# Kernel tuning notes

Measured on AMD Instinct MI355X. Metric: run time of the kernel, lower is better.

## Reference

```python
import jax, jax.numpy as jnp
import numpy as np

B, C, H, W, S = 32, 512, 32, 32, 4
HW = H * W
OUT = HW // S  # conv1/conv2 out channels = 256
EPS = 1e-5


def setup_inputs() -> dict:
    key = jax.random.key(0)
    ks = jax.random.split(key, 8)
    d = {}
    d["x"] = jax.random.normal(ks[0], (B, C, H, W), jnp.float32)
    # conv1 / bn1 (operate on x_flat with 'channels' = h*w)
    d["w1"] = jax.random.normal(ks[1], (OUT, HW), jnp.float32) * 0.02
    d["b1"] = jnp.zeros((OUT,), jnp.float32)
    d["g1"] = jnp.ones((OUT,), jnp.float32)
    d["be1"] = jnp.zeros((OUT,), jnp.float32)
    d["m1"] = jax.random.normal(ks[2], (OUT,), jnp.float32) * 0.01
    d["v1"] = jnp.ones((OUT,), jnp.float32)
    # conv2 / bn2
    d["w2"] = jax.random.normal(ks[3], (OUT, HW), jnp.float32) * 0.02
    d["b2"] = jnp.zeros((OUT,), jnp.float32)
    d["g2"] = jnp.ones((OUT,), jnp.float32)
    d["be2"] = jnp.zeros((OUT,), jnp.float32)
    d["m2"] = jax.random.normal(ks[4], (OUT,), jnp.float32) * 0.01
    d["v2"] = jnp.ones((OUT,), jnp.float32)
    # conv3 / bn3 (1x1 conv on the real channel dim c)
    d["w3"] = jax.random.normal(ks[5], (C, C), jnp.float32) * 0.02
    d["b3"] = jnp.zeros((C,), jnp.float32)
    d["g3"] = jnp.ones((C,), jnp.float32)
    d["be3"] = jnp.zeros((C,), jnp.float32)
    d["m3"] = jax.random.normal(ks[6], (C,), jnp.float32) * 0.01
    d["v3"] = jnp.ones((C,), jnp.float32)
    # conv4: 1x1 conv mapping 1+2c channels -> 1
    d["w4"] = jax.random.normal(ks[7], (1 + 2 * C,), jnp.float32) * 0.02
    d["b4"] = jnp.zeros((), jnp.float32)
    return d


def _bn1d(t, g, be, m, v):
    # t: [b, o, c]; BatchNorm (eval mode) over channel axis 1
    scale = g / jnp.sqrt(v + EPS)
    return (t - m[:, None]) * scale[:, None] + be[:, None]


def reference(x, w1, b1, g1, be1, m1, v1,
              w2, b2, g2, be2, m2, v2,
              w3, b3, g3, be3, m3, v3,
              w4, b4):
    b, c, h, w = x.shape
    # x_flat: [b, h*w, c] -- conv1/conv2 are 1x1 convs over 'channels' = h*w
    xf = x.reshape(b, c, h * w).transpose(0, 2, 1)
    theta = jax.nn.relu(_bn1d(jnp.einsum('oq,bqc->boc', w1, xf) + b1[:, None],
                              g1, be1, m1, v1))  # [b, OUT, c]
    phi = jax.nn.relu(_bn1d(jnp.einsum('oq,bqc->boc', w2, xf) + b2[:, None],
                            g2, be2, m2, v2))    # [b, OUT, c]
    # per-batch conv2d-as-matmul loop collapses to one batched GEMM:
    # affinity[b, i, j] = sum_k phi[b, k, i] * theta[b, k, j]
    aff = jnp.einsum('bki,bkj->bij', phi, theta)  # [b, c, c]
    # x_embed: 1x1 conv + BN + ReLU + global average pool -> [b, c]
    scale3 = g3 / jnp.sqrt(v3 + EPS)
    xe = jnp.einsum('oc,bchw->bohw', w3, x) + b3[:, None, None]
    xe = jax.nn.relu((xe - m3[:, None, None]) * scale3[:, None, None]
                     + be3[:, None, None])
    xe = xe.mean(axis=(2, 3))  # [b, c]
    # conv4 over y = cat([x_embed, affinity_a, affinity_b], dim=1):
    # affinity_a[b,i,0,p] = aff[b,i,p]; affinity_b[b,i,0,p] = aff[b,p,i]
    logits = (w4[0] * xe
              + jnp.einsum('i,bip->bp', w4[1:1 + c], aff)
              + jnp.einsum('i,bpi->bp', w4[1 + c:], aff)
              + b4)
    a = jax.nn.sigmoid(logits)  # [b, c]
    return x * a[:, :, None, None]
```

## Files before the change

kernel.cpp:

```cpp
#include <hip/hip_runtime.h>
#include <math.h>

#define BB   32
#define CC   512
#define HWW  1024
#define OUTC 256
#define EPSV 1e-5f

typedef __attribute__((ext_vector_type(8))) short bfrag;
typedef __attribute__((ext_vector_type(4))) float f32x4;
typedef __attribute__((ext_vector_type(4))) unsigned int u32x4;

__device__ inline unsigned short f2bf(float x){
  unsigned int uu = __float_as_uint(x);
  uu += 0x7fff + ((uu >> 16) & 1);
  return (unsigned short)(uu >> 16);
}
__device__ inline float bf2f(unsigned short h){
  return __uint_as_float(((unsigned int)h) << 16);
}
__device__ inline void packpair(float v0, float v1, unsigned int& hw, unsigned int& lw){
  unsigned short h0 = f2bf(v0), h1 = f2bf(v1);
  unsigned short l0 = f2bf(v0 - bf2f(h0)), l1 = f2bf(v1 - bf2f(h1));
  hw = (unsigned int)h0 | ((unsigned int)h1 << 16);
  lw = (unsigned int)l0 | ((unsigned int)l1 << 16);
}

#define ASYNC16(g, l) \
  __builtin_amdgcn_global_load_lds((const __attribute__((address_space(1))) unsigned int*)(g), \
                                   (__attribute__((address_space(3))) unsigned int*)(l), 16, 0, 0)
#define WAITV(N) asm volatile("s_waitcnt vmcnt(" #N ")" ::: "memory")


__global__ __launch_bounds__(256) void prep(
    const float* __restrict__ x,
    const float* __restrict__ w1, const float* __restrict__ w2,
    const float* __restrict__ w3,
    unsigned short* __restrict__ Xhi, unsigned short* __restrict__ Xlo,
    unsigned short* __restrict__ XThi,
    unsigned short* __restrict__ Whi, unsigned short* __restrict__ Wlo,
    unsigned short* __restrict__ W3hi,
    float* __restrict__ accz)
{
  const int tid = threadIdx.x;
  if (blockIdx.z == 32) {
    int worker = (blockIdx.y * 16 + blockIdx.x) * 256 + tid;
    accz[worker] = 0.f;
#pragma unroll
    for (int s = 0; s < 2; ++s) {
      int cid  = worker * 2 + s;
      int tile = cid >> 6, l = cid & 63;
      int o = (tile >> 5) * 16 + (l & 15);
      int k = (tile & 31) * 32 + (l >> 4) * 8;
      const float* src = (o < 256) ? (w1 + (size_t)o * 1024 + k)
                                   : (w2 + (size_t)(o - 256) * 1024 + k);
      u32x4 hv, lv;
#pragma unroll
      for (int j = 0; j < 4; ++j) {
        unsigned int hw, lw;
        packpair(src[2 * j], src[2 * j + 1], hw, lw);
        hv[j] = hw; lv[j] = lw;
      }
      size_t base = (size_t)tile * 512 + (size_t)l * 8;
      *(u32x4*)(Whi + base) = hv;
      *(u32x4*)(Wlo + base) = lv;
    }
    {
      int tile = worker >> 6, l = worker & 63;
      int o = (tile >> 4) * 16 + (l & 15);
      int c = (tile & 15) * 32 + (l >> 4) * 8;
      const float* src = w3 + (size_t)o * 512 + c;
      u32x4 hv;
#pragma unroll
      for (int j = 0; j < 4; ++j) {
        unsigned short h0 = f2bf(src[2 * j]), h1 = f2bf(src[2 * j + 1]);
        hv[j] = (unsigned int)h0 | ((unsigned int)h1 << 16);
      }
      *(u32x4*)(W3hi + (size_t)tile * 512 + (size_t)l * 8) = hv;
    }
    return;
  }
  __shared__ float T[64][65];
  const int b = blockIdx.z, c0 = blockIdx.y * 64, p0 = blockIdx.x * 64;
  const int tr = tid >> 4, tc4 = (tid & 15) * 4;
  const float* xb = x + (size_t)b * 524288;
#pragma unroll
  for (int r = 0; r < 4; ++r) {
    int cl = tr + r * 16;
    float4 v = *(const float4*)(xb + (size_t)(c0 + cl) * 1024 + p0 + tc4);
    T[cl][tc4 + 0] = v.x; T[cl][tc4 + 1] = v.y;
    T[cl][tc4 + 2] = v.z; T[cl][tc4 + 3] = v.w;
  }
  __syncthreads();
#pragma unroll
  for (int s = 0; s < 2; ++s) {
    int cid  = tid + s * 256;
    int tile = cid >> 6, l = cid & 63;
    int tileC = tile >> 1, tileP = tile & 1;
    int cl = tileC * 16 + (l & 15);
    int pl = tileP * 32 + (l >> 4) * 8;
    u32x4 hv, lv;
#pragma unroll
    for (int j = 0; j < 4; ++j) {
      unsigned int hw, lw;
      packpair(T[cl][pl + 2 * j], T[cl][pl + 2 * j + 1], hw, lw);
      hv[j] = hw; lv[j] = lw;
    }
    size_t base = (size_t)b * 524288
                + ((size_t)((c0 + cl) >> 4) * 32 + (size_t)((p0 + pl) >> 5)) * 512
                + (size_t)l * 8;
    *(u32x4*)(Xhi + base) = hv;
    *(u32x4*)(Xlo + base) = lv;
  }
#pragma unroll
  for (int s = 0; s < 2; ++s) {
    int cid  = tid + s * 256;
    int tile = cid >> 6, l = cid & 63;
    int tileP = tile >> 1, tileC = tile & 1;
    int pl = tileP * 16 + (l & 15);
    int cl = tileC * 32 + (l >> 4) * 8;
    u32x4 hv;
#pragma unroll
    for (int j = 0; j < 4; ++j) {
      unsigned short h0 = f2bf(T[cl + 2 * j][pl]);
      unsigned short h1 = f2bf(T[cl + 2 * j + 1][pl]);
      hv[j] = (unsigned int)h0 | ((unsigned int)h1 << 16);
    }
    size_t base = (size_t)b * 524288
                + ((size_t)((p0 + pl) >> 4) * 16 + (size_t)((c0 + cl) >> 5)) * 512
                + (size_t)l * 8;
    *(u32x4*)(XThi + base) = hv;
  }
}

__global__ __launch_bounds__(256, 2) void gemm_fused(
    const unsigned short* __restrict__ Xhi, const unsigned short* __restrict__ Xlo,
    const unsigned short* __restrict__ Whi, const unsigned short* __restrict__ Wlo,
    const unsigned short* __restrict__ W3hi, const unsigned short* __restrict__ XThi,
    const float* __restrict__ b1p, const float* __restrict__ g1p,
    const float* __restrict__ be1p, const float* __restrict__ m1p, const float* __restrict__ v1p,
    const float* __restrict__ b2p, const float* __restrict__ g2p,
    const float* __restrict__ be2p, const float* __restrict__ m2p, const float* __restrict__ v2p,
    const float* __restrict__ b3p, const float* __restrict__ g3p,
    const float* __restrict__ be3p, const float* __restrict__ m3p, const float* __restrict__ v3p,
    const float* __restrict__ w4,
    float* __restrict__ P2, float* __restrict__ u, float* __restrict__ t,
    float* __restrict__ xe_acc)
{
  __shared__ unsigned short smem[32768];
  const int fid  = blockIdx.x;
  const int tid  = threadIdx.x;
  const int wave = tid >> 6, lane = tid & 63;
  const int fr = lane & 15, fq = lane >> 4;

  if (fid < 512) {
    const int xcd = fid & 7;
    const int n0  = ((fid >> 3) & 3) * 128;
    const int bc  = ((fid >> 5) << 3) | xcd;
    const int b   = bc >> 2;
    const int c0  = (bc & 3) * 128;
    const int wm = wave & 1, wn = wave >> 1;

    const unsigned short* gsrc;
    int ldst;
    if (wave == 0)      { gsrc = Xhi + (size_t)b * 524288 + (size_t)(c0 >> 4) * 16384; ldst = 0; }
    else if (wave == 1) { gsrc = Xlo + (size_t)b * 524288 + (size_t)(c0 >> 4) * 16384; ldst = 4096; }
    else if (wave == 2) { gsrc = Whi + (size_t)(n0 >> 4) * 16384; ldst = 8192; }
    else                { gsrc = Wlo + (size_t)(n0 >> 4) * 16384; ldst = 12288; }
    gsrc += (size_t)lane * 8;

    f32x4 acc[4][4];
    const f32x4 zz = {0.f, 0.f, 0.f, 0.f};
#pragma unroll
    for (int i = 0; i < 4; ++i)
#pragma unroll
      for (int j = 0; j < 4; ++j) acc[i][j] = zz;

#pragma unroll
    for (int i = 0; i < 8; ++i)
      ASYNC16(gsrc + (size_t)i * 16384, smem + ldst + i * 512);

    int cur = 0;
    for (int kq = 0; kq < 32; ++kq) {
      __builtin_amdgcn_sched_barrier(0);
      if (kq + 1 < 32) {
        unsigned short* nb = smem + (cur ^ 1) * 16384 + ldst;
#pragma unroll
        for (int i = 0; i < 8; ++i)
          ASYNC16(gsrc + (size_t)i * 16384 + (kq + 1) * 512, nb + i * 512);
        WAITV(8);
      } else {
        WAITV(0);
      }
      __builtin_amdgcn_s_barrier();
      __builtin_amdgcn_sched_barrier(0);

      const unsigned short* bufc = smem + cur * 16384;
      bfrag ah[4], al[4], bh[4], bl[4];
#pragma unroll
      for (int i = 0; i < 4; ++i) {
        ah[i] = *(const bfrag*)&bufc[(wm * 4 + i) * 512 + lane * 8];
        al[i] = *(const bfrag*)&bufc[4096 + (wm * 4 + i) * 512 + lane * 8];
      }
#pragma unroll
      for (int j = 0; j < 4; ++j) {
        bh[j] = *(const bfrag*)&bufc[8192 + (wn * 4 + j) * 512 + lane * 8];
        bl[j] = *(const bfrag*)&bufc[12288 + (wn * 4 + j) * 512 + lane * 8];
      }
#pragma unroll
      for (int i = 0; i < 4; ++i)
#pragma unroll
        for (int j = 0; j < 4; ++j) {
          acc[i][j] = __builtin_amdgcn_mfma_f32_16x16x32_bf16(ah[i], bh[j], acc[i][j], 0, 0, 0);
          acc[i][j] = __builtin_amdgcn_mfma_f32_16x16x32_bf16(ah[i], bl[j], acc[i][j], 0, 0, 0);
          acc[i][j] = __builtin_amdgcn_mfma_f32_16x16x32_bf16(al[i], bh[j], acc[i][j], 0, 0, 0);
        }
      __builtin_amdgcn_sched_barrier(0);
      __builtin_amdgcn_s_barrier();
      cur ^= 1;
    }
    __builtin_amdgcn_sched_barrier(0);

    const float *bias, *gg, *bes, *mm, *vv_; int cof;
    if (n0 < 256) { bias = b1p; gg = g1p; bes = be1p; mm = m1p; vv_ = v1p; cof = 0; }
    else          { bias = b2p; gg = g2p; bes = be2p; mm = m2p; vv_ = v2p; cof = 256; }
    const float* wsel = (n0 < 256) ? (w4 + 513) : (w4 + 1);
    float* dsel = (n0 < 256) ? (t + b * 256) : (u + b * 256);
    const int cobase = (n0 - cof) + wn * 64;
    float wt[4][4];
#pragma unroll
    for (int i = 0; i < 4; ++i)
#pragma unroll
      for (int r = 0; r < 4; ++r)
        wt[i][r] = wsel[c0 + wm * 64 + i * 16 + fq * 4 + r];

#pragma unroll
    for (int j = 0; j < 4; ++j) {
      int co = n0 + wn * 64 + j * 16 + fr;
      int q = co - cof;
      float s  = gg[q] * rsqrtf(vv_[q] + EPSV);
      float sh = (bias[q] - mm[q]) * s + bes[q];
      float psum = 0.f;
#pragma unroll
      for (int i = 0; i < 4; ++i) {
        int crow = c0 + wm * 64 + i * 16 + fq * 4;
        float* dst = P2 + ((size_t)b * 512 + crow) * 512 + co;
#pragma unroll
        for (int r = 0; r < 4; ++r) {
          float val = fmaxf(acc[i][j][r] * s + sh, 0.f);
          dst[(size_t)r * 512] = val;
          psum += wt[i][r] * val;
        }
      }
      psum += __shfl_xor(psum, 16);
      psum += __shfl_xor(psum, 32);
      if (fq == 0) atomicAdd(&dsel[cobase + j * 16 + fr], psum);
    }
  } else {
    const int h  = fid - 512;
    const int n0 = (h & 7) * 128;
    const int m0 = ((h >> 3) & 3) * 128;
    const int b  = h >> 5;
    const int wm = wave & 1, wn = wave >> 1;

    const unsigned short* gsrc;
    int ldst;
    if (wave < 2) { gsrc = W3hi + (size_t)((m0 >> 4) + wave * 4) * 8192; ldst = wave * 2048; }
    else { gsrc = XThi + (size_t)b * 524288 + (size_t)((n0 >> 4) + (wave - 2) * 4) * 8192;
           ldst = 4096 + (wave - 2) * 2048; }
    gsrc += (size_t)lane * 8;

    f32x4 acc[4][4];
    const f32x4 zz = {0.f, 0.f, 0.f, 0.f};
#pragma unroll
    for (int i = 0; i < 4; ++i)
#pragma unroll
      for (int j = 0; j < 4; ++j) acc[i][j] = zz;

#pragma unroll
    for (int i = 0; i < 4; ++i)
      ASYNC16(gsrc + (size_t)i * 8192, smem + ldst + i * 512);

    int cur = 0;
    for (int kq = 0; kq < 16; ++kq) {
      __builtin_amdgcn_sched_barrier(0);
      if (kq + 1 < 16) {
        unsigned short* nb = smem + (cur ^ 1) * 8192 + ldst;
#pragma unroll
        for (int i = 0; i < 4; ++i)
          ASYNC16(gsrc + (size_t)i * 8192 + (kq + 1) * 512, nb + i * 512);
        WAITV(4);
      } else {
        WAITV(0);
      }
      __builtin_amdgcn_s_barrier();
      __builtin_amdgcn_sched_barrier(0);

      const unsigned short* bufc = smem + cur * 8192;
      bfrag af[4], bf4[4];
#pragma unroll
      for (int i = 0; i < 4; ++i)
        af[i] = *(const bfrag*)&bufc[(wm * 4 + i) * 512 + lane * 8];
#pragma unroll
      for (int j = 0; j < 4; ++j)
        bf4[j] = *(const bfrag*)&bufc[4096 + (wn * 4 + j) * 512 + lane * 8];
#pragma unroll
      for (int i = 0; i < 4; ++i)
#pragma unroll
        for (int j = 0; j < 4; ++j)
          acc[i][j] = __builtin_amdgcn_mfma_f32_16x16x32_bf16(af[i], bf4[j], acc[i][j], 0, 0, 0);
      __builtin_amdgcn_sched_barrier(0);
      __builtin_amdgcn_s_barrier();
      cur ^= 1;
    }
    __builtin_amdgcn_sched_barrier(0);

#pragma unroll
    for (int i = 0; i < 4; ++i) {
#pragma unroll
      for (int r = 0; r < 4; ++r) {
        int o = m0 + wm * 64 + i * 16 + fq * 4 + r;
        float s  = g3p[o] * rsqrtf(v3p[o] + EPSV);
        float sh = (b3p[o] - m3p[o]) * s + be3p[o];
        float v = fmaxf(acc[i][0][r] * s + sh, 0.f) + fmaxf(acc[i][1][r] * s + sh, 0.f)
                + fmaxf(acc[i][2][r] * s + sh, 0.f) + fmaxf(acc[i][3][r] * s + sh, 0.f);
        v += __shfl_xor(v, 1); v += __shfl_xor(v, 2);
        v += __shfl_xor(v, 4); v += __shfl_xor(v, 8);
        if (fr == 0) atomicAdd(&xe_acc[b * 512 + o], v);
      }
    }
  }
}

__global__ __launch_bounds__(256) void k4_gate_out(
    const float* __restrict__ P2, const float* __restrict__ u,
    const float* __restrict__ t, const float* __restrict__ xe_acc,
    const float* __restrict__ w4, const float* __restrict__ b4,
    const float* __restrict__ x, float* __restrict__ out)
{
  __shared__ float us[256], ts[256];
  const int b = blockIdx.x;
  us[threadIdx.x] = u[b * 256 + threadIdx.x];
  ts[threadIdx.x] = t[b * 256 + threadIdx.x];
  __syncthreads();
  const int wave = threadIdx.x >> 6, lane = threadIdx.x & 63;
  const int p = blockIdx.y * 4 + wave;
  const float* row = P2 + ((size_t)b * 512 + p) * 512;
  float4 th = *(const float4*)&row[lane * 4];
  float4 ph = *(const float4*)&row[256 + lane * 4];
  int ki = lane * 4;
  float rs = th.x * us[ki] + th.y * us[ki + 1] + th.z * us[ki + 2] + th.w * us[ki + 3]
           + ph.x * ts[ki] + ph.y * ts[ki + 1] + ph.z * ts[ki + 2] + ph.w * ts[ki + 3];
  rs += __shfl_xor(rs, 1);  rs += __shfl_xor(rs, 2);  rs += __shfl_xor(rs, 4);
  rs += __shfl_xor(rs, 8);  rs += __shfl_xor(rs, 16); rs += __shfl_xor(rs, 32);
  float xe = xe_acc[b * 512 + p] * (1.f / 1024.f);
  float logit = w4[0] * xe + rs + b4[0];
  float a = 1.f / (1.f + expf(-logit));
  const float4* xr = (const float4*)(x + ((size_t)b * 512 + p) * 1024);
  float4* orow = (float4*)(out + ((size_t)b * 512 + p) * 1024);
#pragma unroll
  for (int r2 = 0; r2 < 4; ++r2) {
    float4 xv = xr[lane + r2 * 64];
    float4 ov; ov.x = xv.x * a; ov.y = xv.y * a; ov.z = xv.z * a; ov.w = xv.w * a;
    orow[lane + r2 * 64] = ov;
  }
}

__global__ __launch_bounds__(256) void k1_theta_phi(
    const float* __restrict__ x,
    const float* __restrict__ w1, const float* __restrict__ b1,
    const float* __restrict__ g1, const float* __restrict__ be1,
    const float* __restrict__ m1, const float* __restrict__ v1,
    const float* __restrict__ w2, const float* __restrict__ b2,
    const float* __restrict__ g2, const float* __restrict__ be2,
    const float* __restrict__ m2, const float* __restrict__ v2,
    float* __restrict__ P)
{
  __shared__ __align__(16) float Ws[32][68];
  __shared__ __align__(16) float Xs[32][68];
  const int b  = blockIdx.z;
  const int o0 = blockIdx.y * 64;
  const int c0 = blockIdx.x * 64;
  const int tid = threadIdx.x;
  const int tx = tid & 15, ty = tid >> 4;
  const float* __restrict__ Wbase = (o0 < OUTC) ? (w1 + (size_t)o0 * HWW)
                                                : (w2 + (size_t)(o0 - OUTC) * HWW);
  const float* __restrict__ xb = x + (size_t)b * CC * HWW;
  float acc[4][4] = {{0.f}};
  for (int k0 = 0; k0 < HWW; k0 += 32) {
#pragma unroll
    for (int r = 0; r < 2; ++r) {
      int id  = tid + (r << 8);
      int row = id >> 3;
      int cg  = (id & 7) << 2;
      float4 wv = *(const float4*)(Wbase + (size_t)row * HWW + k0 + cg);
      Ws[cg+0][row] = wv.x; Ws[cg+1][row] = wv.y; Ws[cg+2][row] = wv.z; Ws[cg+3][row] = wv.w;
      float4 xv = *(const float4*)(xb + (size_t)(c0 + row) * HWW + k0 + cg);
      Xs[cg+0][row] = xv.x; Xs[cg+1][row] = xv.y; Xs[cg+2][row] = xv.z; Xs[cg+3][row] = xv.w;
    }
    __syncthreads();
#pragma unroll
    for (int k = 0; k < 32; ++k) {
      float4 av = *(const float4*)&Ws[k][ty * 4];
      float4 bv = *(const float4*)&Xs[k][tx * 4];
      acc[0][0] += av.x*bv.x; acc[0][1] += av.x*bv.y; acc[0][2] += av.x*bv.z; acc[0][3] += av.x*bv.w;
      acc[1][0] += av.y*bv.x; acc[1][1] += av.y*bv.y; acc[1][2] += av.y*bv.z; acc[1][3] += av.y*bv.w;
      acc[2][0] += av.z*bv.x; acc[2][1] += av.z*bv.y; acc[2][2] += av.z*bv.z; acc[2][3] += av.z*bv.w;
      acc[3][0] += av.w*bv.x; acc[3][1] += av.w*bv.y; acc[3][2] += av.w*bv.z; acc[3][3] += av.w*bv.w;
    }
    __syncthreads();
  }
  const float *bias, *g, *be, *m, *v; int ob;
  if (o0 < OUTC) { bias = b1; g = g1; be = be1; m = m1; v = v1; ob = o0; }
  else           { bias = b2; g = g2; be = be2; m = m2; v = v2; ob = o0 - OUTC; }
#pragma unroll
  for (int i = 0; i < 4; ++i) {
    int oi = ob + ty * 4 + i;
    float sc = g[oi] * rsqrtf(v[oi] + EPSV);
    float sh = be[oi] - m[oi] * sc;
    float bb = bias[oi];
    float4 ov;
    ov.x = fmaxf((acc[i][0] + bb) * sc + sh, 0.f);
    ov.y = fmaxf((acc[i][1] + bb) * sc + sh, 0.f);
    ov.z = fmaxf((acc[i][2] + bb) * sc + sh, 0.f);
    ov.w = fmaxf((acc[i][3] + bb) * sc + sh, 0.f);
    int oo = o0 + ty * 4 + i;
    *(float4*)(P + ((size_t)b * 512 + oo) * 512 + c0 + tx * 4) = ov;
  }
}

__global__ __launch_bounds__(256) void k2_xe(
    const float* __restrict__ x, const float* __restrict__ w3,
    const float* __restrict__ b3, const float* __restrict__ g3,
    const float* __restrict__ be3, const float* __restrict__ m3,
    const float* __restrict__ v3, float* __restrict__ xe_acc)
{
  __shared__ __align__(16) float As[32][68];
  __shared__ __align__(16) float Bs[32][68];
  const int b  = blockIdx.z;
  const int o0 = blockIdx.y * 64;
  const int p0 = blockIdx.x * 64;
  const int tid = threadIdx.x;
  const int tx = tid & 15, ty = tid >> 4;
  const float* __restrict__ xb = x + (size_t)b * CC * HWW;
  float acc[4][4] = {{0.f}};
  for (int ck = 0; ck < CC; ck += 32) {
#pragma unroll
    for (int r = 0; r < 2; ++r) {
      int id  = tid + (r << 8);
      int row = id >> 3;
      int cg  = (id & 7) << 2;
      float4 wv = *(const float4*)(w3 + (size_t)(o0 + row) * CC + ck + cg);
      As[cg+0][row] = wv.x; As[cg+1][row] = wv.y; As[cg+2][row] = wv.z; As[cg+3][row] = wv.w;
      int brow = id >> 4;
      int pg   = (id & 15) << 2;
      float4 xv = *(const float4*)(xb + (size_t)(ck + brow) * HWW + p0 + pg);
      *(float4*)&Bs[brow][pg] = xv;
    }
    __syncthreads();
#pragma unroll
    for (int k = 0; k < 32; ++k) {
      float4 av = *(const float4*)&As[k][ty * 4];
      float4 bv = *(const float4*)&Bs[k][tx * 4];
      acc[0][0] += av.x*bv.x; acc[0][1] += av.x*bv.y; acc[0][2] += av.x*bv.z; acc[0][3] += av.x*bv.w;
      acc[1][0] += av.y*bv.x; acc[1][1] += av.y*bv.y; acc[1][2] += av.y*bv.z; acc[1][3] += av.y*bv.w;
      acc[2][0] += av.z*bv.x; acc[2][1] += av.z*bv.y; acc[2][2] += av.z*bv.z; acc[2][3] += av.z*bv.w;
      acc[3][0] += av.w*bv.x; acc[3][1] += av.w*bv.y; acc[3][2] += av.w*bv.z; acc[3][3] += av.w*bv.w;
    }
    __syncthreads();
  }
#pragma unroll
  for (int i = 0; i < 4; ++i) {
    int oo = o0 + ty * 4 + i;
    float sc = g3[oo] * rsqrtf(v3[oo] + EPSV);
    float sh = be3[oo] - m3[oo] * sc;
    float bb = b3[oo];
    float ps = fmaxf((acc[i][0] + bb) * sc + sh, 0.f)
             + fmaxf((acc[i][1] + bb) * sc + sh, 0.f)
             + fmaxf((acc[i][2] + bb) * sc + sh, 0.f)
             + fmaxf((acc[i][3] + bb) * sc + sh, 0.f);
    ps += __shfl_xor(ps, 1);
    ps += __shfl_xor(ps, 2);
    ps += __shfl_xor(ps, 4);
    ps += __shfl_xor(ps, 8);
    if (tx == 0) atomicAdd(&xe_acc[b * CC + oo], ps);
  }
}

__global__ __launch_bounds__(256) void k3_ut(
    const float* __restrict__ P, const float* __restrict__ w4,
    float* __restrict__ u, float* __restrict__ t)
{
  const int b = blockIdx.x;
  const int wv = threadIdx.x >> 6, lane = threadIdx.x & 63;
  const int k = blockIdx.y * 4 + wv;
  const float* __restrict__ w4a = w4 + 1;
  const float* __restrict__ w4b = w4 + 1 + CC;
  const float* __restrict__ throw_ = P + ((size_t)b * 512 + k) * 512;
  const float* __restrict__ phrow  = P + ((size_t)b * 512 + 256 + k) * 512;
  float su = 0.f, st = 0.f;
#pragma unroll
  for (int i = lane; i < CC; i += 64) {
    su += w4a[i] * phrow[i];
    st += w4b[i] * throw_[i];
  }
#pragma unroll
  for (int off = 32; off > 0; off >>= 1) {
    su += __shfl_down(su, off);
    st += __shfl_down(st, off);
  }
  if (lane == 0) { u[b * OUTC + k] = su; t[b * OUTC + k] = st; }
}

__global__ __launch_bounds__(256) void k4_gate(
    const float* __restrict__ P, const float* __restrict__ u,
    const float* __restrict__ t, const float* __restrict__ xe_acc,
    const float* __restrict__ w4, const float* __restrict__ b4,
    float* __restrict__ amul)
{
  __shared__ float us[256], ts[256];
  const int b = blockIdx.x;
  const int p = blockIdx.y * 256 + threadIdx.x;
  us[threadIdx.x] = u[b * OUTC + threadIdx.x];
  ts[threadIdx.x] = t[b * OUTC + threadIdx.x];
  __syncthreads();
  const float* __restrict__ theta = P + (size_t)b * 512 * 512;
  const float* __restrict__ phi   = theta + 256 * 512;
  float r = 0.f, s = 0.f;
#pragma unroll 8
  for (int k = 0; k < OUTC; ++k) {
    r += us[k] * theta[(size_t)k * 512 + p];
    s += ts[k] * phi[(size_t)k * 512 + p];
  }
  float xe = xe_acc[b * CC + p] * (1.0f / 1024.0f);
  float logit = w4[0] * xe + r + s + b4[0];
  amul[b * CC + p] = 1.0f / (1.0f + expf(-logit));
}

__global__ __launch_bounds__(256) void k5_out(
    const float* __restrict__ x, const float* __restrict__ amul,
    float* __restrict__ out)
{
  int i = blockIdx.x * 256 + threadIdx.x;
  float4 xv = ((const float4*)x)[i];
  float a = amul[i >> 8];
  float4 ov; ov.x = xv.x * a; ov.y = xv.y * a; ov.z = xv.z * a; ov.w = xv.w * a;
  ((float4*)out)[i] = ov;
}

extern "C" void kernel_launch(void* const* d_in, const int* in_sizes, int n_in,
                              void* d_out, int out_size, void* d_ws, size_t ws_size,
                              hipStream_t stream)
{
  (void)in_sizes; (void)n_in; (void)out_size;
  const float* x   = (const float*)d_in[0];
  const float* w1  = (const float*)d_in[1];
  const float* b1  = (const float*)d_in[2];
  const float* g1  = (const float*)d_in[3];
  const float* be1 = (const float*)d_in[4];
  const float* m1  = (const float*)d_in[5];
  const float* v1  = (const float*)d_in[6];
  const float* w2  = (const float*)d_in[7];
  const float* b2  = (const float*)d_in[8];
  const float* g2  = (const float*)d_in[9];
  const float* be2 = (const float*)d_in[10];
  const float* m2  = (const float*)d_in[11];
  const float* v2  = (const float*)d_in[12];
  const float* w3  = (const float*)d_in[13];
  const float* b3  = (const float*)d_in[14];
  const float* g3  = (const float*)d_in[15];
  const float* be3 = (const float*)d_in[16];
  const float* m3  = (const float*)d_in[17];
  const float* v3  = (const float*)d_in[18];
  const float* w4  = (const float*)d_in[19];
  const float* b4  = (const float*)d_in[20];
  float* out = (float*)d_out;

  if (ws_size >= 136970240ull) {
    float* P2     = (float*)d_ws;
    float* xe_acc = P2 + 8388608;
    float* u      = P2 + 8404992;
    float* t      = P2 + 8413184;
    unsigned short* Xhi  = (unsigned short*)((char*)d_ws + 33685504);
    unsigned short* Xlo  = Xhi + 16777216;
    unsigned short* XThi = Xlo + 16777216;
    unsigned short* Whi  = XThi + 16777216;
    unsigned short* Wlo  = Whi + 524288;
    unsigned short* W3hi = Wlo + 524288;

    prep<<<dim3(16, 8, 33), 256, 0, stream>>>(x, w1, w2, w3, Xhi, Xlo, XThi,
                                              Whi, Wlo, W3hi, xe_acc);
    gemm_fused<<<dim3(1536), 256, 0, stream>>>(Xhi, Xlo, Whi, Wlo, W3hi, XThi,
        b1, g1, be1, m1, v1, b2, g2, be2, m2, v2, b3, g3, be3, m3, v3,
        w4, P2, u, t, xe_acc);
    k4_gate_out<<<dim3(32, 128), 256, 0, stream>>>(P2, u, t, xe_acc, w4, b4, x, out);
  } else {
    float* P      = (float*)d_ws;
    float* xe_acc = P + (size_t)BB * 512 * 512;
    float* u      = xe_acc + BB * CC;
    float* t      = u + BB * OUTC;
    float* amul   = t + BB * OUTC;

    hipMemsetAsync(xe_acc, 0, (size_t)BB * CC * sizeof(float), stream);

    dim3 blk(256);
    k1_theta_phi<<<dim3(8, 8, BB), blk, 0, stream>>>(x, w1, b1, g1, be1, m1, v1,
                                                     w2, b2, g2, be2, m2, v2, P);
    k2_xe<<<dim3(16, 8, BB), blk, 0, stream>>>(x, w3, b3, g3, be3, m3, v3, xe_acc);
    k3_ut<<<dim3(BB, 64), blk, 0, stream>>>(P, w4, u, t);
    k4_gate<<<dim3(BB, 2), blk, 0, stream>>>(P, u, t, xe_acc, w4, b4, amul);
    k5_out<<<dim3((BB * CC * HWW / 4) / 256), blk, 0, stream>>>(x, amul, out);
  }
}
```

Before: 257.4 us.

## Load weight fragments directly to registers, stage only activations in LDS

In both GEMM branches the weight operand (W hi/lo, W3) is no longer staged through shared memory. Each wave now loads its own fragments straight from global memory into registers, double-buffered across two k-steps. Only the activation tiles still go through LDS, so shared memory per block halves and the loop is manually unrolled by two with fixed buffers. The aim is less LDS traffic and capacity and more blocks resident per CU. The cost is more VGPR pressure and weight data read redundantly from global/L2 by waves that share a column tile.

```diff
diff --git a/kernel.cpp b/kernel.cpp
--- a/kernel.cpp
+++ b/kernel.cpp
@@ -147,7 +147,7 @@
     float* __restrict__ P2, float* __restrict__ u, float* __restrict__ t,
     float* __restrict__ xe_acc)
 {
-  __shared__ unsigned short smem[32768];
+  __shared__ unsigned short smem[16384];
   const int fid  = blockIdx.x;
   const int tid  = threadIdx.x;
   const int wave = tid >> 6, lane = tid & 63;
@@ -161,13 +161,13 @@
     const int c0  = (bc & 3) * 128;
     const int wm = wave & 1, wn = wave >> 1;
 
-    const unsigned short* gsrc;
-    int ldst;
-    if (wave == 0)      { gsrc = Xhi + (size_t)b * 524288 + (size_t)(c0 >> 4) * 16384; ldst = 0; }
-    else if (wave == 1) { gsrc = Xlo + (size_t)b * 524288 + (size_t)(c0 >> 4) * 16384; ldst = 4096; }
-    else if (wave == 2) { gsrc = Whi + (size_t)(n0 >> 4) * 16384; ldst = 8192; }
-    else                { gsrc = Wlo + (size_t)(n0 >> 4) * 16384; ldst = 12288; }
-    gsrc += (size_t)lane * 8;
+    const unsigned short* gAh = Xhi + (size_t)b * 524288
+        + (size_t)((c0 >> 4) + 2 * wave) * 16384 + (size_t)lane * 8;
+    const unsigned short* gAl = Xlo + (size_t)b * 524288
+        + (size_t)((c0 >> 4) + 2 * wave) * 16384 + (size_t)lane * 8;
+
+    const bfrag* Bh = (const bfrag*)Whi + (size_t)((n0 >> 4) + wn * 4) * 2048 + lane;
+    const bfrag* Bl = (const bfrag*)Wlo + (size_t)((n0 >> 4) + wn * 4) * 2048 + lane;
 
     f32x4 acc[4][4];
     const f32x4 zz = {0.f, 0.f, 0.f, 0.f};
@@ -176,48 +176,91 @@
 #pragma unroll
       for (int j = 0; j < 4; ++j) acc[i][j] = zz;
 
-#pragma unroll
-    for (int i = 0; i < 8; ++i)
-      ASYNC16(gsrc + (size_t)i * 16384, smem + ldst + i * 512);
-
-    int cur = 0;
-    for (int kq = 0; kq < 32; ++kq) {
-      __builtin_amdgcn_sched_barrier(0);
-      if (kq + 1 < 32) {
-        unsigned short* nb = smem + (cur ^ 1) * 16384 + ldst;
-#pragma unroll
-        for (int i = 0; i < 8; ++i)
-          ASYNC16(gsrc + (size_t)i * 16384 + (kq + 1) * 512, nb + i * 512);
-        WAITV(8);
+    bfrag bhA[4], blA[4], bhB[4], blB[4];
+#pragma unroll
+    for (int j = 0; j < 4; ++j) {
+      bhA[j] = Bh[(size_t)j * 2048];
+      blA[j] = Bl[(size_t)j * 2048];
+    }
+    __builtin_amdgcn_sched_barrier(0);
+#pragma unroll
+    for (int ti = 0; ti < 2; ++ti) {
+      ASYNC16(gAh + (size_t)ti * 16384, smem + (2 * wave + ti) * 512);
+      ASYNC16(gAl + (size_t)ti * 16384, smem + 4096 + (2 * wave + ti) * 512);
+    }
+
+    for (int kq = 0; kq < 32; kq += 2) {
+      __builtin_amdgcn_sched_barrier(0);
+#pragma unroll
+      for (int j = 0; j < 4; ++j) {
+        bhB[j] = Bh[(size_t)j * 2048 + (kq + 1) * 64];
+        blB[j] = Bl[(size_t)j * 2048 + (kq + 1) * 64];
+      }
+      __builtin_amdgcn_sched_barrier(0);
+#pragma unroll
+      for (int ti = 0; ti < 2; ++ti) {
+        ASYNC16(gAh + (size_t)ti * 16384 + (kq + 1) * 512, smem + 8192 + (2 * wave + ti) * 512);
+        ASYNC16(gAl + (size_t)ti * 16384 + (kq + 1) * 512, smem + 12288 + (2 * wave + ti) * 512);
+      }
+      WAITV(12);
+      __builtin_amdgcn_s_barrier();
+      __builtin_amdgcn_sched_barrier(0);
+      {
+        bfrag ah[4], al[4];
+#pragma unroll
+        for (int i = 0; i < 4; ++i) {
+          ah[i] = *(const bfrag*)&smem[(wm * 4 + i) * 512 + lane * 8];
+          al[i] = *(const bfrag*)&smem[4096 + (wm * 4 + i) * 512 + lane * 8];
+        }
+#pragma unroll
+        for (int i = 0; i < 4; ++i)
+#pragma unroll
+          for (int j = 0; j < 4; ++j) {
+            acc[i][j] = __builtin_amdgcn_mfma_f32_16x16x32_bf16(ah[i], bhA[j], acc[i][j], 0, 0, 0);
+            acc[i][j] = __builtin_amdgcn_mfma_f32_16x16x32_bf16(ah[i], blA[j], acc[i][j], 0, 0, 0);
+            acc[i][j] = __builtin_amdgcn_mfma_f32_16x16x32_bf16(al[i], bhA[j], acc[i][j], 0, 0, 0);
+          }
+      }
+      __builtin_amdgcn_sched_barrier(0);
+      __builtin_amdgcn_s_barrier();
+
+      __builtin_amdgcn_sched_barrier(0);
+      if (kq + 2 < 32) {
+#pragma unroll
+        for (int j = 0; j < 4; ++j) {
+          bhA[j] = Bh[(size_t)j * 2048 + (kq + 2) * 64];
+          blA[j] = Bl[(size_t)j * 2048 + (kq + 2) * 64];
+        }
+        __builtin_amdgcn_sched_barrier(0);
+#pragma unroll
+        for (int ti = 0; ti < 2; ++ti) {
+          ASYNC16(gAh + (size_t)ti * 16384 + (kq + 2) * 512, smem + (2 * wave + ti) * 512);
+          ASYNC16(gAl + (size_t)ti * 16384 + (kq + 2) * 512, smem + 4096 + (2 * wave + ti) * 512);
+        }
+        WAITV(12);
       } else {
         WAITV(0);
       }
       __builtin_amdgcn_s_barrier();
       __builtin_amdgcn_sched_barrier(0);
-
-      const unsigned short* bufc = smem + cur * 16384;
-      bfrag ah[4], al[4], bh[4], bl[4];
-#pragma unroll
-      for (int i = 0; i < 4; ++i) {
-        ah[i] = *(const bfrag*)&bufc[(wm * 4 + i) * 512 + lane * 8];
-        al[i] = *(const bfrag*)&bufc[4096 + (wm * 4 + i) * 512 + lane * 8];
-      }
-#pragma unroll
-      for (int j = 0; j < 4; ++j) {
-        bh[j] = *(const bfrag*)&bufc[8192 + (wn * 4 + j) * 512 + lane * 8];
-        bl[j] = *(const bfrag*)&bufc[12288 + (wn * 4 + j) * 512 + lane * 8];
-      }
-#pragma unroll
-      for (int i = 0; i < 4; ++i)
-#pragma unroll
-        for (int j = 0; j < 4; ++j) {
-          acc[i][j] = __builtin_amdgcn_mfma_f32_16x16x32_bf16(ah[i], bh[j], acc[i][j], 0, 0, 0);
-          acc[i][j] = __builtin_amdgcn_mfma_f32_16x16x32_bf16(ah[i], bl[j], acc[i][j], 0, 0, 0);
-          acc[i][j] = __builtin_amdgcn_mfma_f32_16x16x32_bf16(al[i], bh[j], acc[i][j], 0, 0, 0);
+      {
+        bfrag ah[4], al[4];
+#pragma unroll
+        for (int i = 0; i < 4; ++i) {
+          ah[i] = *(const bfrag*)&smem[8192 + (wm * 4 + i) * 512 + lane * 8];
+          al[i] = *(const bfrag*)&smem[12288 + (wm * 4 + i) * 512 + lane * 8];
         }
-      __builtin_amdgcn_sched_barrier(0);
-      __builtin_amdgcn_s_barrier();
-      cur ^= 1;
+#pragma unroll
+        for (int i = 0; i < 4; ++i)
+#pragma unroll
+          for (int j = 0; j < 4; ++j) {
+            acc[i][j] = __builtin_amdgcn_mfma_f32_16x16x32_bf16(ah[i], bhB[j], acc[i][j], 0, 0, 0);
+            acc[i][j] = __builtin_amdgcn_mfma_f32_16x16x32_bf16(ah[i], blB[j], acc[i][j], 0, 0, 0);
+            acc[i][j] = __builtin_amdgcn_mfma_f32_16x16x32_bf16(al[i], bhB[j], acc[i][j], 0, 0, 0);
+          }
+      }
+      __builtin_amdgcn_sched_barrier(0);
+      __builtin_amdgcn_s_barrier();
     }
     __builtin_amdgcn_sched_barrier(0);
 
@@ -263,12 +306,9 @@
     const int b  = h >> 5;
     const int wm = wave & 1, wn = wave >> 1;
 
-    const unsigned short* gsrc;
-    int ldst;
-    if (wave < 2) { gsrc = W3hi + (size_t)((m0 >> 4) + wave * 4) * 8192; ldst = wave * 2048; }
-    else { gsrc = XThi + (size_t)b * 524288 + (size_t)((n0 >> 4) + (wave - 2) * 4) * 8192;
-           ldst = 4096 + (wave - 2) * 2048; }
-    gsrc += (size_t)lane * 8;
+    const unsigned short* gB = XThi + (size_t)b * 524288
+        + (size_t)((n0 >> 4) + 2 * wave) * 8192 + (size_t)lane * 8;
+    const bfrag* Af = (const bfrag*)W3hi + (size_t)((m0 >> 4) + wm * 4) * 1024 + lane;
 
     f32x4 acc[4][4];
     const f32x4 zz = {0.f, 0.f, 0.f, 0.f};
@@ -277,41 +317,66 @@
 #pragma unroll
       for (int j = 0; j < 4; ++j) acc[i][j] = zz;
 
-#pragma unroll
-    for (int i = 0; i < 4; ++i)
-      ASYNC16(gsrc + (size_t)i * 8192, smem + ldst + i * 512);
-
-    int cur = 0;
-    for (int kq = 0; kq < 16; ++kq) {
-      __builtin_amdgcn_sched_barrier(0);
-      if (kq + 1 < 16) {
-        unsigned short* nb = smem + (cur ^ 1) * 8192 + ldst;
+    bfrag afA[4], afB[4];
+#pragma unroll
+    for (int i = 0; i < 4; ++i) afA[i] = Af[(size_t)i * 1024];
+    __builtin_amdgcn_sched_barrier(0);
+#pragma unroll
+    for (int ti = 0; ti < 2; ++ti)
+      ASYNC16(gB + (size_t)ti * 8192, smem + (2 * wave + ti) * 512);
+
+    for (int kq = 0; kq < 16; kq += 2) {
+      __builtin_amdgcn_sched_barrier(0);
+#pragma unroll
+      for (int i = 0; i < 4; ++i) afB[i] = Af[(size_t)i * 1024 + (kq + 1) * 64];
+      __builtin_amdgcn_sched_barrier(0);
+#pragma unroll
+      for (int ti = 0; ti < 2; ++ti)
+        ASYNC16(gB + (size_t)ti * 8192 + (kq + 1) * 512, smem + 4096 + (2 * wave + ti) * 512);
+      WAITV(6);
+      __builtin_amdgcn_s_barrier();
+      __builtin_amdgcn_sched_barrier(0);
+      {
+        bfrag bf4[4];
+#pragma unroll
+        for (int j = 0; j < 4; ++j)
+          bf4[j] = *(const bfrag*)&smem[(wn * 4 + j) * 512 + lane * 8];
 #pragma unroll
         for (int i = 0; i < 4; ++i)
-          ASYNC16(gsrc + (size_t)i * 8192 + (kq + 1) * 512, nb + i * 512);
-        WAITV(4);
+#pragma unroll
+          for (int j = 0; j < 4; ++j)
+            acc[i][j] = __builtin_amdgcn_mfma_f32_16x16x32_bf16(afA[i], bf4[j], acc[i][j], 0, 0, 0);
+      }
+      __builtin_amdgcn_sched_barrier(0);
+      __builtin_amdgcn_s_barrier();
+
+      __builtin_amdgcn_sched_barrier(0);
+      if (kq + 2 < 16) {
+#pragma unroll
+        for (int i = 0; i < 4; ++i) afA[i] = Af[(size_t)i * 1024 + (kq + 2) * 64];
+        __builtin_amdgcn_sched_barrier(0);
+#pragma unroll
+        for (int ti = 0; ti < 2; ++ti)
+          ASYNC16(gB + (size_t)ti * 8192 + (kq + 2) * 512, smem + (2 * wave + ti) * 512);
+        WAITV(6);
       } else {
         WAITV(0);
       }
       __builtin_amdgcn_s_barrier();
       __builtin_amdgcn_sched_barrier(0);
-
-      const unsigned short* bufc = smem + cur * 8192;
-      bfrag af[4], bf4[4];
-#pragma unroll
-      for (int i = 0; i < 4; ++i)
-        af[i] = *(const bfrag*)&bufc[(wm * 4 + i) * 512 + lane * 8];
-#pragma unroll
-      for (int j = 0; j < 4; ++j)
-        bf4[j] = *(const bfrag*)&bufc[4096 + (wn * 4 + j) * 512 + lane * 8];
-#pragma unroll
-      for (int i = 0; i < 4; ++i)
+      {
+        bfrag bf4[4];
 #pragma unroll
         for (int j = 0; j < 4; ++j)
-          acc[i][j] = __builtin_amdgcn_mfma_f32_16x16x32_bf16(af[i], bf4[j], acc[i][j], 0, 0, 0);
-      __builtin_amdgcn_sched_barrier(0);
-      __builtin_amdgcn_s_barrier();
-      cur ^= 1;
+          bf4[j] = *(const bfrag*)&smem[4096 + (wn * 4 + j) * 512 + lane * 8];
+#pragma unroll
+        for (int i = 0; i < 4; ++i)
+#pragma unroll
+          for (int j = 0; j < 4; ++j)
+            acc[i][j] = __builtin_amdgcn_mfma_f32_16x16x32_bf16(afB[i], bf4[j], acc[i][j], 0, 0, 0);
+      }
+      __builtin_amdgcn_sched_barrier(0);
+      __builtin_amdgcn_s_barrier();
     }
     __builtin_amdgcn_sched_barrier(0);
 
```

After: 262.0 us. Within noise of the previous version (+1.8%).
